# Kernel tuning notes

Hardware: AMD Instinct MI355X
Metric: run time of the kernel (lower is better)

Reference implementation:

```python
import jax, jax.numpy as jnp
import numpy as np

# dimensions
B, NQ, D, H, L, KT, KF = 4, 8192, 256, 8, 4, 2, 2
K = KT * KF
DH = D // H
SPATIAL = np.array([[64, 64], [32, 32], [16, 16], [8, 8]], dtype=np.int32)  # (H_l, W_l)
_sizes = SPATIAL[:, 0] * SPATIAL[:, 1]
LSI = np.concatenate([[0], np.cumsum(_sizes)[:-1]]).astype(np.int32)
NV = int(_sizes.sum())


def setup_inputs() -> dict:
    key = jax.random.key(0)
    ks = jax.random.split(key, 12)
    s = 0.02  # small weight scale keeps tanh in linear region like the zero-init original
    # biases per _reset_parameters: +-0.5 grid for offsets, level-specialization for level_weights
    b_time = jnp.asarray(np.tile(np.linspace(-0.5, 0.5, KT), H * L).astype(np.float32))
    b_freq = jnp.asarray(np.tile(np.linspace(-0.5, 0.5, KF).astype(np.float32), H * L))
    lvl_bias = np.zeros((H, L), dtype=np.float32)
    hpl = max(1, H // L)
    for lvl in range(L):
        lvl_bias[lvl * hpl:min(lvl * hpl + hpl, H), lvl] = 1.0
    return dict(
        query=jax.random.normal(ks[0], (B, NQ, D), jnp.float32),
        reference_points=jax.random.uniform(ks[1], (B, NQ, L, 2), jnp.float32),
        value=jax.random.normal(ks[2], (B, NV, D), jnp.float32),
        spatial_shapes=jnp.asarray(SPATIAL),
        level_start_index=jnp.asarray(LSI),
        W_time=jax.random.normal(ks[3], (D, H * L * KT), jnp.float32) * s,
        b_time=b_time,
        W_freq=jax.random.normal(ks[4], (D, H * L * KF), jnp.float32) * s,
        b_freq=b_freq,
        W_lvl=jax.random.normal(ks[5], (D, H * L), jnp.float32) * s,
        b_lvl=jnp.asarray(lvl_bias.reshape(-1)),
        W_pt=jax.random.normal(ks[6], (D, H * L * K), jnp.float32) * s,
        b_pt=jnp.zeros((H * L * K,), jnp.float32),
        W_v=jax.random.normal(ks[7], (D, D), jnp.float32) * (1.0 / np.sqrt(D)),
        b_v=jnp.zeros((D,), jnp.float32),
        W_o=jax.random.normal(ks[8], (D, D), jnp.float32) * (1.0 / np.sqrt(D)),
        b_o=jnp.zeros((D,), jnp.float32),
    )


def _bilinear(vlev, gx, gy, Hl, Wl):
    # vlev: [B,H,Hl*Wl,DH]; gx,gy: [B,H,NQ,K] normalized grid coords in [-1,1]
    # F.grid_sample(align_corners=False, padding_mode='zeros') semantics
    x = (gx + 1.0) * (Wl * 0.5) - 0.5
    y = (gy + 1.0) * (Hl * 0.5) - 0.5
    x0 = jnp.floor(x)
    y0 = jnp.floor(y)
    wx1 = x - x0
    wy1 = y - y0
    x0i = x0.astype(jnp.int32)
    y0i = y0.astype(jnp.int32)

    def gather(xi, yi, w):
        valid = (xi >= 0) & (xi < Wl) & (yi >= 0) & (yi < Hl)
        idx = jnp.clip(yi, 0, Hl - 1) * Wl + jnp.clip(xi, 0, Wl - 1)
        b, h, nq, k = idx.shape
        v = jnp.take_along_axis(vlev, idx.reshape(b, h, nq * k)[..., None], axis=2)
        v = v.reshape(b, h, nq, k, DH)
        return v * (w * valid)[..., None]

    return (gather(x0i, y0i, (1.0 - wx1) * (1.0 - wy1))
            + gather(x0i + 1, y0i, wx1 * (1.0 - wy1))
            + gather(x0i, y0i + 1, (1.0 - wx1) * wy1)
            + gather(x0i + 1, y0i + 1, wx1 * wy1))


def _forward(query, reference_points, value, W_time, b_time, W_freq, b_freq,
             W_lvl, b_lvl, W_pt, b_pt, W_v, b_v, W_o, b_o,
             spatial_shapes, level_start_index):
    ss = np.asarray(spatial_shapes)
    lsi = np.asarray(level_start_index)
    # predicted separable offsets (offset_scale = 1.0)
    t_off = jnp.tanh(query @ W_time + b_time).reshape(B, NQ, H, L, KT)
    f_off = jnp.tanh(query @ W_freq + b_freq).reshape(B, NQ, H, L, KF)
    # square grid: outer product of time (x) and freq (y) offsets -> K = KT*KF points
    off = jnp.stack([
        jnp.broadcast_to(t_off[..., :, None], (B, NQ, H, L, KT, KF)),
        jnp.broadcast_to(f_off[..., None, :], (B, NQ, H, L, KT, KF)),
    ], axis=-1).reshape(B, NQ, H, L, K, 2)
    # normalizer: (W_l, H_l) per level
    norm = jnp.stack([spatial_shapes[:, 1], spatial_shapes[:, 0]], axis=-1).astype(jnp.float32)
    loc = reference_points[:, :, None, :, None, :] + off / norm[None, None, None, :, None, :]
    loc = jnp.clip(loc, 0.0, 1.0)
    grid = 2.0 * loc - 1.0  # [B,NQ,H,L,K,2], last dim = (x, y)
    # attention weights: softmax over levels times softmax over points
    lw = jax.nn.softmax((query @ W_lvl + b_lvl).reshape(B, NQ, H, L), axis=-1)
    pw = jax.nn.softmax((query @ W_pt + b_pt).reshape(B, NQ, H, L, K), axis=-1)
    attn = lw[..., None] * pw  # [B,NQ,H,L,K]
    v = (value @ W_v + b_v).reshape(B, NV, H, DH)
    out = jnp.zeros((B, NQ, H, DH), jnp.float32)
    for lid in range(L):
        Hl, Wl = int(ss[lid, 0]), int(ss[lid, 1])
        start = int(lsi[lid])
        vlev = v[:, start:start + Hl * Wl].transpose(0, 2, 1, 3)  # [B,H,S_l,DH]
        gx = grid[:, :, :, lid, :, 0].transpose(0, 2, 1, 3)  # [B,H,NQ,K]
        gy = grid[:, :, :, lid, :, 1].transpose(0, 2, 1, 3)
        sampled = _bilinear(vlev, gx, gy, Hl, Wl)  # [B,H,NQ,K,DH]
        a = attn[:, :, :, lid, :].transpose(0, 2, 1, 3)  # [B,H,NQ,K]
        out = out + jnp.einsum('bhqkd,bhqk->bqhd', sampled, a)
    out = out.reshape(B, NQ, D)
    return out @ W_o + b_o


def reference(query, reference_points, value, spatial_shapes, level_start_index,
              W_time, b_time, W_freq, b_freq, W_lvl, b_lvl, W_pt, b_pt,
              W_v, b_v, W_o, b_o):
    return _forward(query, reference_points, value, W_time, b_time, W_freq, b_freq,
                    W_lvl, b_lvl, W_pt, b_pt, W_v, b_v, W_o, b_o,
                    spatial_shapes, level_start_index)
```

## Files before the change

kernel.cpp:

```cpp
#include <hip/hip_runtime.h>
#include <math.h>

#define B_  4
#define NQ_ 8192
#define D_  256
#define H_  8
#define L_  4
#define K_  4
#define DH_ 32
#define NV_ 5440

#define SLAB_ 5936

typedef short bf16x8 __attribute__((ext_vector_type(8)));
typedef float f32x4  __attribute__((ext_vector_type(4)));
typedef unsigned short u16x8 __attribute__((ext_vector_type(8)));

__device__ __forceinline__ ushort f2bf(float f) {
    union { float f; unsigned u; } v; v.f = f;
    return (ushort)((v.u + 0x7FFF + ((v.u >> 16) & 1)) >> 16);
}
__device__ __forceinline__ float bf2f(ushort u) {
    union { unsigned u; float f; } v; v.u = ((unsigned)u) << 16;
    return v.f;
}

__global__ __launch_bounds__(256) void k_zero(uint4* __restrict__ p) {
    p[(size_t)blockIdx.x * 256 + threadIdx.x] = make_uint4(0, 0, 0, 0);
}

__global__ __launch_bounds__(256) void k_cvta(const float* __restrict__ in,
                                              ushort* __restrict__ out) {
    const size_t base = ((size_t)blockIdx.x * 256 + threadIdx.x) * 8;
    const float4 a = *(const float4*)(in + base);
    const float4 b = *(const float4*)(in + base + 4);
    u16x8 u;
    u[0] = f2bf(a.x); u[1] = f2bf(a.y); u[2] = f2bf(a.z); u[3] = f2bf(a.w);
    u[4] = f2bf(b.x); u[5] = f2bf(b.y); u[6] = f2bf(b.z); u[7] = f2bf(b.w);
    *(u16x8*)(out + base) = u;
}

__global__ __launch_bounds__(256) void k_cvtw(const float* __restrict__ in,
                                              ushort* __restrict__ out) {
    const int n = blockIdx.x, k = threadIdx.x;
    out[n * 256 + k] = f2bf(in[k * 256 + n]);
}

__global__ __launch_bounds__(256) void k_cvtwq(const float* __restrict__ Wt,
                                               const float* __restrict__ Wf,
                                               const float* __restrict__ Wlv,
                                               const float* __restrict__ Wp,
                                               ushort* __restrict__ out) {
    const int n = blockIdx.x, k = threadIdx.x;
    float v;
    if (n < 64)       v = Wt[k * 64 + n];
    else if (n < 128) v = Wf[k * 64 + (n - 64)];
    else if (n < 160) v = Wlv[k * 32 + (n - 128)];
    else              v = Wp[k * 128 + (n - 160)];
    out[n * 256 + k] = f2bf(v);
}

template<int NT, int MODE, int AF32>
__global__ __launch_bounds__(256) void k_gemm(const void* __restrict__ Ap,
                                              const ushort* __restrict__ Bt,
                                              const float* __restrict__ bias,
                                              void* __restrict__ Cp) {
    constexpr int NFN = NT / 32;
    __shared__ ushort As[128 * 32];
    __shared__ ushort Bs[NT * 32];
    const int m0   = blockIdx.x * 128;
    const int n0   = blockIdx.y * NT;
    const int t    = threadIdx.x;
    const int w    = t >> 6;
    const int lane = t & 63;
    const int wm   = (w >> 1) * 64;
    const int wn   = (w & 1) * (NT / 2);
    const int lm   = lane & 15;
    const int quad = lane >> 4;

    f32x4 acc[4][NFN];
    #pragma unroll
    for (int i = 0; i < 4; ++i)
        #pragma unroll
        for (int j = 0; j < NFN; ++j)
            acc[i][j] = (f32x4)(0.f);

    for (int kc = 0; kc < 256; kc += 32) {
        __syncthreads();
        if (AF32) {
            const float* A = (const float*)Ap;
            #pragma unroll
            for (int i = 0; i < 4; ++i) {
                const int c   = t + i * 256;
                const int row = c >> 3, ko = (c & 7) * 4;
                const float4 v = *(const float4*)&A[(size_t)(m0 + row) * 256 + kc + ko];
                ushort4 u; u.x = f2bf(v.x); u.y = f2bf(v.y); u.z = f2bf(v.z); u.w = f2bf(v.w);
                *(ushort4*)&As[row * 32 + ko] = u;
            }
        } else {
            const ushort* A = (const ushort*)Ap;
            #pragma unroll
            for (int i = 0; i < 2; ++i) {
                const int c   = t + i * 256;
                const int row = c >> 2, ko = (c & 3) * 8;
                *(u16x8*)&As[row * 32 + ko] =
                    *(const u16x8*)&A[(size_t)(m0 + row) * 256 + kc + ko];
            }
        }
        #pragma unroll
        for (int i = 0; i < 2; ++i) {
            const int c = t + i * 256;
            if (NT == 128 || c < NT * 4) {
                const int row = c >> 2, ko = (c & 3) * 8;
                *(u16x8*)&Bs[row * 32 + ko] =
                    *(const u16x8*)&Bt[(size_t)(n0 + row) * 256 + kc + ko];
            }
        }
        __syncthreads();

        bf16x8 af[4], bfr[NFN];
        #pragma unroll
        for (int mf = 0; mf < 4; ++mf)
            af[mf] = *(const bf16x8*)&As[(wm + mf * 16 + lm) * 32 + quad * 8];
        #pragma unroll
        for (int nf = 0; nf < NFN; ++nf)
            bfr[nf] = *(const bf16x8*)&Bs[(wn + nf * 16 + lm) * 32 + quad * 8];
        #pragma unroll
        for (int mf = 0; mf < 4; ++mf)
            #pragma unroll
            for (int nf = 0; nf < NFN; ++nf)
                acc[mf][nf] = __builtin_amdgcn_mfma_f32_16x16x32_bf16(
                    af[mf], bfr[nf], acc[mf][nf], 0, 0, 0);
    }

    #pragma unroll
    for (int mf = 0; mf < 4; ++mf) {
        #pragma unroll
        for (int nf = 0; nf < NFN; ++nf) {
            const f32x4 a = acc[mf][nf];
            const int col   = n0 + wn + nf * 16 + lm;
            const int rbase = m0 + wm + mf * 16 + quad * 4;
            #pragma unroll
            for (int r = 0; r < 4; ++r) {
                const int row = rbase + r;
                const float v = a[r];
                if (MODE == 0) {
                    ((float*)Cp)[(size_t)row * 256 + col] = v + bias[col];
                } else if (MODE == 1) {
                    const int b = row / NV_, s = row - b * NV_;
                    const int h = col >> 5, dh = col & 31;
                    const int l = (s >= 5376) ? 3 : (s >= 5120) ? 2 : (s >= 4096) ? 1 : 0;
                    const int lsi_[4] = {0, 4096, 5120, 5376};
                    const int po_[4]  = {0, 4356, 5512, 5836};
                    const int o  = s - lsi_[l];
                    const int Wl = 64 >> l;
                    const int y  = o >> (6 - l);
                    const int x  = o & (Wl - 1);
                    const int prow = po_[l] + (y + 1) * (Wl + 2) + (x + 1);
                    ((ushort*)Cp)[(((size_t)(b * H_ + h)) * SLAB_ + prow) * 32 + dh] =
                        f2bf(v + bias[col]);
                } else {
                    ((float*)Cp)[(size_t)row * 288 + col] = v;
                }
            }
        }
    }
}

__global__ __launch_bounds__(256) void k_epi(const float* __restrict__ logits,
                                             const float* __restrict__ refpts,
                                             const float* __restrict__ bt,
                                             const float* __restrict__ bfq,
                                             const float* __restrict__ blv,
                                             const float* __restrict__ bp,
                                             float* __restrict__ params) {
    const int item = blockIdx.x * 256 + threadIdx.x;
    const int qg = item >> 5;
    const int hl = item & 31;
    const int h = hl >> 2, l = hl & 3;
    const float* lgr = logits + (size_t)qg * 288;

    const float tA = tanhf(lgr[hl * 2 + 0] + bt[hl * 2 + 0]);
    const float tB = tanhf(lgr[hl * 2 + 1] + bt[hl * 2 + 1]);
    const float fA = tanhf(lgr[64 + hl * 2 + 0] + bfq[hl * 2 + 0]);
    const float fB = tanhf(lgr[64 + hl * 2 + 1] + bfq[hl * 2 + 1]);

    const float l0 = lgr[128 + h * 4 + 0] + blv[h * 4 + 0];
    const float l1 = lgr[128 + h * 4 + 1] + blv[h * 4 + 1];
    const float l2 = lgr[128 + h * 4 + 2] + blv[h * 4 + 2];
    const float l3 = lgr[128 + h * 4 + 3] + blv[h * 4 + 3];
    const float lm = fmaxf(fmaxf(l0, l1), fmaxf(l2, l3));
    const float e0 = __expf(l0 - lm), e1 = __expf(l1 - lm);
    const float e2 = __expf(l2 - lm), e3 = __expf(l3 - lm);
    const float lsum = e0 + e1 + e2 + e3;
    const float lwv = ((l == 0) ? e0 : (l == 1) ? e1 : (l == 2) ? e2 : e3) / lsum;

    const float p0 = lgr[160 + hl * 4 + 0] + bp[hl * 4 + 0];
    const float p1 = lgr[160 + hl * 4 + 1] + bp[hl * 4 + 1];
    const float p2 = lgr[160 + hl * 4 + 2] + bp[hl * 4 + 2];
    const float p3 = lgr[160 + hl * 4 + 3] + bp[hl * 4 + 3];
    const float pmx = fmaxf(fmaxf(p0, p1), fmaxf(p2, p3));
    const float q0e = __expf(p0 - pmx), q1e = __expf(p1 - pmx);
    const float q2e = __expf(p2 - pmx), q3e = __expf(p3 - pmx);
    const float inv = lwv / (q0e + q1e + q2e + q3e);

    const float rx = refpts[((size_t)qg * L_ + l) * 2 + 0];
    const float ry = refpts[((size_t)qg * L_ + l) * 2 + 1];
    const float Wlf = (float)(64 >> l);
    const float Hlf = (float)(64 >> l);
    const float xA = fminf(fmaxf(rx + tA / Wlf, 0.f), 1.f) * Wlf - 0.5f;
    const float xB = fminf(fmaxf(rx + tB / Wlf, 0.f), 1.f) * Wlf - 0.5f;
    const float yA = fminf(fmaxf(ry + fA / Hlf, 0.f), 1.f) * Hlf - 0.5f;
    const float yB = fminf(fmaxf(ry + fB / Hlf, 0.f), 1.f) * Hlf - 0.5f;

    float* pp = params + (size_t)qg * 256 + hl * 8;
    pp[0] = q0e * inv; pp[1] = q1e * inv; pp[2] = q2e * inv; pp[3] = q3e * inv;
    pp[4] = xA; pp[5] = xB; pp[6] = yA; pp[7] = yB;
}

__global__ __launch_bounds__(256) void k_sample(const ushort* __restrict__ vperm,
                                                const float* __restrict__ params,
                                                ushort* __restrict__ mid) {
    __shared__ float pm[8][264];
    const int b   = blockIdx.y;
    const int q0  = blockIdx.x * 8;
    const int t   = threadIdx.x;
    const int qs  = t >> 6;
    const int sub = t & 63;
    const int h   = sub >> 3;
    const int dh4 = sub & 7;

    for (int i = t; i < 8 * 256; i += 256) {
        const int q = i >> 8, c = i & 255;
        pm[q][(c >> 5) * 33 + (c & 31)] = params[((size_t)(b * NQ_ + q0 + q)) * 256 + c];
    }
    __syncthreads();

    const ushort* vb = vperm + ((size_t)(b * H_ + h)) * SLAB_ * 32 + dh4 * 4;
    const int po_[4] = {0, 4356, 5512, 5836};

    #pragma unroll
    for (int i = 0; i < 2; ++i) {
        const int ql = qs + i * 4;
        f32x4 acc = (f32x4)(0.f);
        #pragma unroll
        for (int l = 0; l < L_; ++l) {
            const int W2 = (64 >> l) + 2;
            const ushort* vl = vb + (size_t)po_[l] * 32;
            const float* p  = &pm[ql][h * 33 + l * 8];
            const float a0 = p[0], a1 = p[1], a2 = p[2], a3 = p[3];
            const float xA = p[4], xB = p[5], yA = p[6], yB = p[7];
            const float xa0 = floorf(xA), xb0 = floorf(xB);
            const float ya0 = floorf(yA), yb0 = floorf(yB);
            const float fxa = xA - xa0, fxb = xB - xb0;
            const float fya = yA - ya0, fyb = yB - yb0;
            const int pxa = (int)xa0 + 1, pxb = (int)xb0 + 1;
            const int pya = (int)ya0 + 1, pyb = (int)yb0 + 1;
            #pragma unroll
            for (int k = 0; k < 4; ++k) {
                const int   px = (k & 2) ? pxb : pxa;
                const int   py = (k & 1) ? pyb : pya;
                const float fx = (k & 2) ? fxb : fxa;
                const float fy = (k & 1) ? fyb : fya;
                const float ak = (k == 0) ? a0 : (k == 1) ? a1 : (k == 2) ? a2 : a3;
                const ushort* c = vl + (size_t)(py * W2 + px) * 32;
                const ushort4 u00 = *(const ushort4*)c;
                const ushort4 u10 = *(const ushort4*)(c + 32);
                const ushort4 u01 = *(const ushort4*)(c + W2 * 32);
                const ushort4 u11 = *(const ushort4*)(c + (W2 + 1) * 32);
                const float gx = 1.f - fx, gy = 1.f - fy;
                const float w00 = ak * gx * gy, w10 = ak * fx * gy;
                const float w01 = ak * gx * fy, w11 = ak * fx * fy;
                f32x4 v;
                v.x = bf2f(u00.x) * w00 + bf2f(u10.x) * w10 + bf2f(u01.x) * w01 + bf2f(u11.x) * w11;
                v.y = bf2f(u00.y) * w00 + bf2f(u10.y) * w10 + bf2f(u01.y) * w01 + bf2f(u11.y) * w11;
                v.z = bf2f(u00.z) * w00 + bf2f(u10.z) * w10 + bf2f(u01.z) * w01 + bf2f(u11.z) * w11;
                v.w = bf2f(u00.w) * w00 + bf2f(u10.w) * w10 + bf2f(u01.w) * w01 + bf2f(u11.w) * w11;
                acc += v;
            }
        }
        ushort4 o;
        o.x = f2bf(acc.x); o.y = f2bf(acc.y); o.z = f2bf(acc.z); o.w = f2bf(acc.w);
        *(ushort4*)&mid[((size_t)(b * NQ_ + q0 + ql)) * 256 + sub * 4] = o;
    }
}

extern "C" void kernel_launch(void* const* d_in, const int* in_sizes, int n_in,
                              void* d_out, int out_size, void* d_ws, size_t ws_size,
                              hipStream_t stream) {
    const float* query = (const float*)d_in[0];
    const float* refp  = (const float*)d_in[1];
    const float* value = (const float*)d_in[2];
    const float* Wt = (const float*)d_in[5];
    const float* bt = (const float*)d_in[6];
    const float* Wf = (const float*)d_in[7];
    const float* bf = (const float*)d_in[8];
    const float* Wl = (const float*)d_in[9];
    const float* bl = (const float*)d_in[10];
    const float* Wp = (const float*)d_in[11];
    const float* bp = (const float*)d_in[12];
    const float* Wv = (const float*)d_in[13];
    const float* bv = (const float*)d_in[14];
    const float* Wo = (const float*)d_in[15];
    const float* bo = (const float*)d_in[16];

    char* wsb = (char*)d_ws;
    ushort* vperm  = (ushort*)wsb;
    float*  params = (float*)(wsb + 12156928);
    ushort* qbf    = (ushort*)(wsb + 12156928);
    float*  logits = (float*)(wsb + 45711360);
    ushort* midb   = (ushort*)(wsb + 45711360);
    ushort* Wvt    = (ushort*)(wsb + 83460096);
    ushort* Wot    = (ushort*)(wsb + 83591168);
    ushort* Wqt    = (ushort*)(wsb + 83722240);

    k_cvtw<<<256, 256, 0, stream>>>(Wv, Wvt);
    k_cvtw<<<256, 256, 0, stream>>>(Wo, Wot);
    k_cvtwq<<<288, 256, 0, stream>>>(Wt, Wf, Wl, Wp, Wqt);
    k_cvta<<<4096, 256, 0, stream>>>(query, qbf);
    k_zero<<<2968, 256, 0, stream>>>((uint4*)vperm);

    k_gemm<128, 1, 1><<<dim3(170, 2), 256, 0, stream>>>(value, Wvt, bv, vperm);
    k_gemm<96, 2, 0><<<dim3(256, 3), 256, 0, stream>>>(qbf, Wqt, nullptr, logits);
    k_epi<<<4096, 256, 0, stream>>>(logits, refp, bt, bf, bl, bp, params);
    k_sample<<<dim3(NQ_ / 8, B_), 256, 0, stream>>>(vperm, params, midb);
    k_gemm<128, 0, 0><<<dim3(256, 2), 256, 0, stream>>>(midb, Wot, bo, (float*)d_out);
}
```

Baseline: 260.4 us.

## Fuse query projection with epilogue, merge prep kernels, widen sampling vectors

Merges the weight conversions and zeroing into one prep kernel, and fuses the query cast, query projection GEMM and softmax/offset epilogue into a single kernel that stages logits in shared memory. This removes the bf16 query buffer and the fp32 logits round trip through global memory, plus several launches. The sampling kernel now has each thread handle 8 channels of one query with 16-byte loads and declares an occupancy hint of 5 blocks. The fused projection uses 64-row tiles with 18 accumulators per wave, which raises register pressure and could lower occupancy.

```diff
diff --git a/kernel.cpp b/kernel.cpp
--- a/kernel.cpp
+++ b/kernel.cpp
@@ -14,6 +14,7 @@
 
 typedef short bf16x8 __attribute__((ext_vector_type(8)));
 typedef float f32x4  __attribute__((ext_vector_type(4)));
+typedef float f32x8  __attribute__((ext_vector_type(8)));
 typedef unsigned short u16x8 __attribute__((ext_vector_type(8)));
 
 __device__ __forceinline__ ushort f2bf(float f) {
@@ -25,47 +26,43 @@
     return v.f;
 }
 
-__global__ __launch_bounds__(256) void k_zero(uint4* __restrict__ p) {
-    p[(size_t)blockIdx.x * 256 + threadIdx.x] = make_uint4(0, 0, 0, 0);
-}
-
-__global__ __launch_bounds__(256) void k_cvta(const float* __restrict__ in,
-                                              ushort* __restrict__ out) {
-    const size_t base = ((size_t)blockIdx.x * 256 + threadIdx.x) * 8;
-    const float4 a = *(const float4*)(in + base);
-    const float4 b = *(const float4*)(in + base + 4);
-    u16x8 u;
-    u[0] = f2bf(a.x); u[1] = f2bf(a.y); u[2] = f2bf(a.z); u[3] = f2bf(a.w);
-    u[4] = f2bf(b.x); u[5] = f2bf(b.y); u[6] = f2bf(b.z); u[7] = f2bf(b.w);
-    *(u16x8*)(out + base) = u;
-}
-
-__global__ __launch_bounds__(256) void k_cvtw(const float* __restrict__ in,
-                                              ushort* __restrict__ out) {
-    const int n = blockIdx.x, k = threadIdx.x;
-    out[n * 256 + k] = f2bf(in[k * 256 + n]);
-}
-
-__global__ __launch_bounds__(256) void k_cvtwq(const float* __restrict__ Wt,
-                                               const float* __restrict__ Wf,
-                                               const float* __restrict__ Wlv,
-                                               const float* __restrict__ Wp,
-                                               ushort* __restrict__ out) {
-    const int n = blockIdx.x, k = threadIdx.x;
-    float v;
-    if (n < 64)       v = Wt[k * 64 + n];
-    else if (n < 128) v = Wf[k * 64 + (n - 64)];
-    else if (n < 160) v = Wlv[k * 32 + (n - 128)];
-    else              v = Wp[k * 128 + (n - 160)];
-    out[n * 256 + k] = f2bf(v);
-}
-
-template<int NT, int MODE, int AF32>
+__global__ __launch_bounds__(256) void k_prep(const float* __restrict__ Wv,
+                                              const float* __restrict__ Wo,
+                                              const float* __restrict__ Wt,
+                                              const float* __restrict__ Wf,
+                                              const float* __restrict__ Wlv,
+                                              const float* __restrict__ Wp,
+                                              uint4* __restrict__ vzero,
+                                              ushort* __restrict__ Wvt,
+                                              ushort* __restrict__ Wot,
+                                              ushort* __restrict__ Wqt) {
+    const int bk = blockIdx.x;
+    const int t  = threadIdx.x;
+    if (bk < 2968) {
+        vzero[(size_t)bk * 256 + t] = make_uint4(0, 0, 0, 0);
+    } else if (bk < 3480) {
+        const float* in; ushort* out; int n;
+        if (bk < 3224) { in = Wv; out = Wvt; n = bk - 2968; }
+        else           { in = Wo; out = Wot; n = bk - 3224; }
+        out[n * 256 + t] = f2bf(in[t * 256 + n]);
+    } else {
+        const int n = bk - 3480;
+        float v;
+        if (n < 64)       v = Wt[t * 64 + n];
+        else if (n < 128) v = Wf[t * 64 + (n - 64)];
+        else if (n < 160) v = Wlv[t * 32 + (n - 128)];
+        else              v = Wp[t * 128 + (n - 160)];
+        Wqt[n * 256 + t] = f2bf(v);
+    }
+}
+
+template<int MODE, int AF32>
 __global__ __launch_bounds__(256) void k_gemm(const void* __restrict__ Ap,
                                               const ushort* __restrict__ Bt,
                                               const float* __restrict__ bias,
                                               void* __restrict__ Cp) {
-    constexpr int NFN = NT / 32;
+    constexpr int NT = 128;
+    constexpr int NFN = 4;
     __shared__ ushort As[128 * 32];
     __shared__ ushort Bs[NT * 32];
     const int m0   = blockIdx.x * 128;
@@ -110,11 +107,9 @@
         #pragma unroll
         for (int i = 0; i < 2; ++i) {
             const int c = t + i * 256;
-            if (NT == 128 || c < NT * 4) {
-                const int row = c >> 2, ko = (c & 3) * 8;
-                *(u16x8*)&Bs[row * 32 + ko] =
-                    *(const u16x8*)&Bt[(size_t)(n0 + row) * 256 + kc + ko];
-            }
+            const int row = c >> 2, ko = (c & 3) * 8;
+            *(u16x8*)&Bs[row * 32 + ko] =
+                *(const u16x8*)&Bt[(size_t)(n0 + row) * 256 + kc + ko];
         }
         __syncthreads();
 
@@ -146,7 +141,7 @@
                 const float v = a[r];
                 if (MODE == 0) {
                     ((float*)Cp)[(size_t)row * 256 + col] = v + bias[col];
-                } else if (MODE == 1) {
+                } else {
                     const int b = row / NV_, s = row - b * NV_;
                     const int h = col >> 5, dh = col & 31;
                     const int l = (s >= 5376) ? 3 : (s >= 5120) ? 2 : (s >= 4096) ? 1 : 0;
@@ -159,76 +154,151 @@
                     const int prow = po_[l] + (y + 1) * (Wl + 2) + (x + 1);
                     ((ushort*)Cp)[(((size_t)(b * H_ + h)) * SLAB_ + prow) * 32 + dh] =
                         f2bf(v + bias[col]);
-                } else {
-                    ((float*)Cp)[(size_t)row * 288 + col] = v;
                 }
             }
         }
     }
 }
 
-__global__ __launch_bounds__(256) void k_epi(const float* __restrict__ logits,
-                                             const float* __restrict__ refpts,
-                                             const float* __restrict__ bt,
-                                             const float* __restrict__ bfq,
-                                             const float* __restrict__ blv,
-                                             const float* __restrict__ bp,
-                                             float* __restrict__ params) {
-    const int item = blockIdx.x * 256 + threadIdx.x;
-    const int qg = item >> 5;
-    const int hl = item & 31;
-    const int h = hl >> 2, l = hl & 3;
-    const float* lgr = logits + (size_t)qg * 288;
-
-    const float tA = tanhf(lgr[hl * 2 + 0] + bt[hl * 2 + 0]);
-    const float tB = tanhf(lgr[hl * 2 + 1] + bt[hl * 2 + 1]);
-    const float fA = tanhf(lgr[64 + hl * 2 + 0] + bfq[hl * 2 + 0]);
-    const float fB = tanhf(lgr[64 + hl * 2 + 1] + bfq[hl * 2 + 1]);
-
-    const float l0 = lgr[128 + h * 4 + 0] + blv[h * 4 + 0];
-    const float l1 = lgr[128 + h * 4 + 1] + blv[h * 4 + 1];
-    const float l2 = lgr[128 + h * 4 + 2] + blv[h * 4 + 2];
-    const float l3 = lgr[128 + h * 4 + 3] + blv[h * 4 + 3];
-    const float lm = fmaxf(fmaxf(l0, l1), fmaxf(l2, l3));
-    const float e0 = __expf(l0 - lm), e1 = __expf(l1 - lm);
-    const float e2 = __expf(l2 - lm), e3 = __expf(l3 - lm);
-    const float lsum = e0 + e1 + e2 + e3;
-    const float lwv = ((l == 0) ? e0 : (l == 1) ? e1 : (l == 2) ? e2 : e3) / lsum;
-
-    const float p0 = lgr[160 + hl * 4 + 0] + bp[hl * 4 + 0];
-    const float p1 = lgr[160 + hl * 4 + 1] + bp[hl * 4 + 1];
-    const float p2 = lgr[160 + hl * 4 + 2] + bp[hl * 4 + 2];
-    const float p3 = lgr[160 + hl * 4 + 3] + bp[hl * 4 + 3];
-    const float pmx = fmaxf(fmaxf(p0, p1), fmaxf(p2, p3));
-    const float q0e = __expf(p0 - pmx), q1e = __expf(p1 - pmx);
-    const float q2e = __expf(p2 - pmx), q3e = __expf(p3 - pmx);
-    const float inv = lwv / (q0e + q1e + q2e + q3e);
-
-    const float rx = refpts[((size_t)qg * L_ + l) * 2 + 0];
-    const float ry = refpts[((size_t)qg * L_ + l) * 2 + 1];
-    const float Wlf = (float)(64 >> l);
-    const float Hlf = (float)(64 >> l);
-    const float xA = fminf(fmaxf(rx + tA / Wlf, 0.f), 1.f) * Wlf - 0.5f;
-    const float xB = fminf(fmaxf(rx + tB / Wlf, 0.f), 1.f) * Wlf - 0.5f;
-    const float yA = fminf(fmaxf(ry + fA / Hlf, 0.f), 1.f) * Hlf - 0.5f;
-    const float yB = fminf(fmaxf(ry + fB / Hlf, 0.f), 1.f) * Hlf - 0.5f;
-
-    float* pp = params + (size_t)qg * 256 + hl * 8;
-    pp[0] = q0e * inv; pp[1] = q1e * inv; pp[2] = q2e * inv; pp[3] = q3e * inv;
-    pp[4] = xA; pp[5] = xB; pp[6] = yA; pp[7] = yB;
-}
-
-__global__ __launch_bounds__(256) void k_sample(const ushort* __restrict__ vperm,
-                                                const float* __restrict__ params,
-                                                ushort* __restrict__ mid) {
+__global__ __launch_bounds__(256) void k_qproj(const float* __restrict__ query,
+                                               const ushort* __restrict__ Wqt,
+                                               const float* __restrict__ refpts,
+                                               const float* __restrict__ bt,
+                                               const float* __restrict__ bfq,
+                                               const float* __restrict__ blv,
+                                               const float* __restrict__ bp,
+                                               float* __restrict__ params) {
+    __shared__ __align__(16) char smem[37888];
+    ushort* As = (ushort*)smem;
+    ushort* Bs = As + 64 * 32;
+    float*  ep = (float*)smem;
+
+    const int m0   = blockIdx.x * 64;
+    const int t    = threadIdx.x;
+    const int w    = t >> 6;
+    const int lane = t & 63;
+    const int wm   = (w >> 1) * 32;
+    const int wn   = (w & 1) * 144;
+    const int lm   = lane & 15;
+    const int quad = lane >> 4;
+
+    f32x4 acc[2][9];
+    #pragma unroll
+    for (int i = 0; i < 2; ++i)
+        #pragma unroll
+        for (int j = 0; j < 9; ++j)
+            acc[i][j] = (f32x4)(0.f);
+
+    for (int kc = 0; kc < 256; kc += 32) {
+        __syncthreads();
+        #pragma unroll
+        for (int i = 0; i < 2; ++i) {
+            const int c   = t + i * 256;
+            const int row = c >> 3, ko = (c & 7) * 4;
+            const float4 v = *(const float4*)&query[(size_t)(m0 + row) * 256 + kc + ko];
+            ushort4 u; u.x = f2bf(v.x); u.y = f2bf(v.y); u.z = f2bf(v.z); u.w = f2bf(v.w);
+            *(ushort4*)&As[row * 32 + ko] = u;
+        }
+        #pragma unroll
+        for (int i = 0; i < 5; ++i) {
+            const int c = t + i * 256;
+            if (c < 1152) {
+                const int row = c >> 2, ko = (c & 3) * 8;
+                *(u16x8*)&Bs[row * 32 + ko] =
+                    *(const u16x8*)&Wqt[(size_t)row * 256 + kc + ko];
+            }
+        }
+        __syncthreads();
+
+        bf16x8 af[2], bfr[9];
+        #pragma unroll
+        for (int mf = 0; mf < 2; ++mf)
+            af[mf] = *(const bf16x8*)&As[(wm + mf * 16 + lm) * 32 + quad * 8];
+        #pragma unroll
+        for (int nf = 0; nf < 9; ++nf)
+            bfr[nf] = *(const bf16x8*)&Bs[(wn + nf * 16 + lm) * 32 + quad * 8];
+        #pragma unroll
+        for (int mf = 0; mf < 2; ++mf)
+            #pragma unroll
+            for (int nf = 0; nf < 9; ++nf)
+                acc[mf][nf] = __builtin_amdgcn_mfma_f32_16x16x32_bf16(
+                    af[mf], bfr[nf], acc[mf][nf], 0, 0, 0);
+    }
+
+    #pragma unroll
+    for (int ph = 0; ph < 2; ++ph) {
+        __syncthreads();
+        if ((w >> 1) == ph) {
+            #pragma unroll
+            for (int mf = 0; mf < 2; ++mf)
+                #pragma unroll
+                for (int nf = 0; nf < 9; ++nf)
+                    #pragma unroll
+                    for (int r = 0; r < 4; ++r)
+                        ep[(mf * 16 + quad * 4 + r) * 296 + wn + nf * 16 + lm]
+                            = acc[mf][nf][r];
+        }
+        __syncthreads();
+        #pragma unroll
+        for (int it = 0; it < 4; ++it) {
+            const int item = t + it * 256;
+            const int qr = item >> 5;
+            const int hl = item & 31;
+            const int h = hl >> 2, l = hl & 3;
+            const int qg = m0 + ph * 32 + qr;
+            const float* lgr = &ep[qr * 296];
+
+            const float tA = tanhf(lgr[hl * 2 + 0] + bt[hl * 2 + 0]);
+            const float tB = tanhf(lgr[hl * 2 + 1] + bt[hl * 2 + 1]);
+            const float fA = tanhf(lgr[64 + hl * 2 + 0] + bfq[hl * 2 + 0]);
+            const float fB = tanhf(lgr[64 + hl * 2 + 1] + bfq[hl * 2 + 1]);
+
+            const float l0 = lgr[128 + h * 4 + 0] + blv[h * 4 + 0];
+            const float l1 = lgr[128 + h * 4 + 1] + blv[h * 4 + 1];
+            const float l2 = lgr[128 + h * 4 + 2] + blv[h * 4 + 2];
+            const float l3 = lgr[128 + h * 4 + 3] + blv[h * 4 + 3];
+            const float lmx = fmaxf(fmaxf(l0, l1), fmaxf(l2, l3));
+            const float e0 = __expf(l0 - lmx), e1 = __expf(l1 - lmx);
+            const float e2 = __expf(l2 - lmx), e3 = __expf(l3 - lmx);
+            const float lsum = e0 + e1 + e2 + e3;
+            const float lwv = ((l == 0) ? e0 : (l == 1) ? e1 : (l == 2) ? e2 : e3) / lsum;
+
+            const float p0 = lgr[160 + hl * 4 + 0] + bp[hl * 4 + 0];
+            const float p1 = lgr[160 + hl * 4 + 1] + bp[hl * 4 + 1];
+            const float p2 = lgr[160 + hl * 4 + 2] + bp[hl * 4 + 2];
+            const float p3 = lgr[160 + hl * 4 + 3] + bp[hl * 4 + 3];
+            const float pmx = fmaxf(fmaxf(p0, p1), fmaxf(p2, p3));
+            const float q0e = __expf(p0 - pmx), q1e = __expf(p1 - pmx);
+            const float q2e = __expf(p2 - pmx), q3e = __expf(p3 - pmx);
+            const float inv = lwv / (q0e + q1e + q2e + q3e);
+
+            const float rx = refpts[((size_t)qg * L_ + l) * 2 + 0];
+            const float ry = refpts[((size_t)qg * L_ + l) * 2 + 1];
+            const float Wlf = (float)(64 >> l);
+            const float Hlf = (float)(64 >> l);
+            const float xA = fminf(fmaxf(rx + tA / Wlf, 0.f), 1.f) * Wlf - 0.5f;
+            const float xB = fminf(fmaxf(rx + tB / Wlf, 0.f), 1.f) * Wlf - 0.5f;
+            const float yA = fminf(fmaxf(ry + fA / Hlf, 0.f), 1.f) * Hlf - 0.5f;
+            const float yB = fminf(fmaxf(ry + fB / Hlf, 0.f), 1.f) * Hlf - 0.5f;
+
+            float* pp = params + (size_t)qg * 256 + hl * 8;
+            pp[0] = q0e * inv; pp[1] = q1e * inv; pp[2] = q2e * inv; pp[3] = q3e * inv;
+            pp[4] = xA; pp[5] = xB; pp[6] = yA; pp[7] = yB;
+        }
+    }
+}
+
+__global__ __launch_bounds__(256, 5) void k_sample(const ushort* __restrict__ vperm,
+                                                   const float* __restrict__ params,
+                                                   ushort* __restrict__ mid) {
     __shared__ float pm[8][264];
     const int b   = blockIdx.y;
     const int q0  = blockIdx.x * 8;
     const int t   = threadIdx.x;
-    const int qs  = t >> 6;
-    const int sub = t & 63;
-    const int h   = sub >> 3;
-    const int dh4 = sub & 7;
+    const int ql  = t >> 5;
+    const int sub = t & 31;
+    const int h   = sub >> 2;
+    const int dh8 = sub & 3;
 
     for (int i = t; i < 8 * 256; i += 256) {
         const int q = i >> 8, c = i & 255;
@@ -236,53 +306,48 @@
     }
     __syncthreads();
 
-    const ushort* vb = vperm + ((size_t)(b * H_ + h)) * SLAB_ * 32 + dh4 * 4;
+    const ushort* vb = vperm + ((size_t)(b * H_ + h)) * SLAB_ * 32 + dh8 * 8;
     const int po_[4] = {0, 4356, 5512, 5836};
 
-    #pragma unroll
-    for (int i = 0; i < 2; ++i) {
-        const int ql = qs + i * 4;
-        f32x4 acc = (f32x4)(0.f);
-        #pragma unroll
-        for (int l = 0; l < L_; ++l) {
-            const int W2 = (64 >> l) + 2;
-            const ushort* vl = vb + (size_t)po_[l] * 32;
-            const float* p  = &pm[ql][h * 33 + l * 8];
-            const float a0 = p[0], a1 = p[1], a2 = p[2], a3 = p[3];
-            const float xA = p[4], xB = p[5], yA = p[6], yB = p[7];
-            const float xa0 = floorf(xA), xb0 = floorf(xB);
-            const float ya0 = floorf(yA), yb0 = floorf(yB);
-            const float fxa = xA - xa0, fxb = xB - xb0;
-            const float fya = yA - ya0, fyb = yB - yb0;
-            const int pxa = (int)xa0 + 1, pxb = (int)xb0 + 1;
-            const int pya = (int)ya0 + 1, pyb = (int)yb0 + 1;
-            #pragma unroll
-            for (int k = 0; k < 4; ++k) {
-                const int   px = (k & 2) ? pxb : pxa;
-                const int   py = (k & 1) ? pyb : pya;
-                const float fx = (k & 2) ? fxb : fxa;
-                const float fy = (k & 1) ? fyb : fya;
-                const float ak = (k == 0) ? a0 : (k == 1) ? a1 : (k == 2) ? a2 : a3;
-                const ushort* c = vl + (size_t)(py * W2 + px) * 32;
-                const ushort4 u00 = *(const ushort4*)c;
-                const ushort4 u10 = *(const ushort4*)(c + 32);
-                const ushort4 u01 = *(const ushort4*)(c + W2 * 32);
-                const ushort4 u11 = *(const ushort4*)(c + (W2 + 1) * 32);
-                const float gx = 1.f - fx, gy = 1.f - fy;
-                const float w00 = ak * gx * gy, w10 = ak * fx * gy;
-                const float w01 = ak * gx * fy, w11 = ak * fx * fy;
-                f32x4 v;
-                v.x = bf2f(u00.x) * w00 + bf2f(u10.x) * w10 + bf2f(u01.x) * w01 + bf2f(u11.x) * w11;
-                v.y = bf2f(u00.y) * w00 + bf2f(u10.y) * w10 + bf2f(u01.y) * w01 + bf2f(u11.y) * w11;
-                v.z = bf2f(u00.z) * w00 + bf2f(u10.z) * w10 + bf2f(u01.z) * w01 + bf2f(u11.z) * w11;
-                v.w = bf2f(u00.w) * w00 + bf2f(u10.w) * w10 + bf2f(u01.w) * w01 + bf2f(u11.w) * w11;
-                acc += v;
-            }
-        }
-        ushort4 o;
-        o.x = f2bf(acc.x); o.y = f2bf(acc.y); o.z = f2bf(acc.z); o.w = f2bf(acc.w);
-        *(ushort4*)&mid[((size_t)(b * NQ_ + q0 + ql)) * 256 + sub * 4] = o;
-    }
+    f32x8 acc = (f32x8)(0.f);
+    #pragma unroll
+    for (int l = 0; l < L_; ++l) {
+        const int W2 = (64 >> l) + 2;
+        const ushort* vl = vb + (size_t)po_[l] * 32;
+        const float* p  = &pm[ql][h * 33 + l * 8];
+        const float a0 = p[0], a1 = p[1], a2 = p[2], a3 = p[3];
+        const float xA = p[4], xB = p[5], yA = p[6], yB = p[7];
+        const float xa0 = floorf(xA), xb0 = floorf(xB);
+        const float ya0 = floorf(yA), yb0 = floorf(yB);
+        const float fxa = xA - xa0, fxb = xB - xb0;
+        const float fya = yA - ya0, fyb = yB - yb0;
+        const int pxa = (int)xa0 + 1, pxb = (int)xb0 + 1;
+        const int pya = (int)ya0 + 1, pyb = (int)yb0 + 1;
+        #pragma unroll
+        for (int k = 0; k < 4; ++k) {
+            const int   px = (k & 2) ? pxb : pxa;
+            const int   py = (k & 1) ? pyb : pya;
+            const float fx = (k & 2) ? fxb : fxa;
+            const float fy = (k & 1) ? fyb : fya;
+            const float ak = (k == 0) ? a0 : (k == 1) ? a1 : (k == 2) ? a2 : a3;
+            const ushort* cp = vl + (size_t)(py * W2 + px) * 32;
+            const u16x8 u00 = *(const u16x8*)cp;
+            const u16x8 u10 = *(const u16x8*)(cp + 32);
+            const u16x8 u01 = *(const u16x8*)(cp + W2 * 32);
+            const u16x8 u11 = *(const u16x8*)(cp + (W2 + 1) * 32);
+            const float gx = 1.f - fx, gy = 1.f - fy;
+            const float w00 = ak * gx * gy, w10 = ak * fx * gy;
+            const float w01 = ak * gx * fy, w11 = ak * fx * fy;
+            #pragma unroll
+            for (int e = 0; e < 8; ++e)
+                acc[e] += bf2f(u00[e]) * w00 + bf2f(u10[e]) * w10
+                        + bf2f(u01[e]) * w01 + bf2f(u11[e]) * w11;
+        }
+    }
+    u16x8 o;
+    #pragma unroll
+    for (int e = 0; e < 8; ++e) o[e] = f2bf(acc[e]);
+    *(u16x8*)&mid[((size_t)(b * NQ_ + q0 + ql)) * 256 + sub * 8] = o;
 }
 
 extern "C" void kernel_launch(void* const* d_in, const int* in_sizes, int n_in,
@@ -307,22 +372,15 @@
     char* wsb = (char*)d_ws;
     ushort* vperm  = (ushort*)wsb;
     float*  params = (float*)(wsb + 12156928);
-    ushort* qbf    = (ushort*)(wsb + 12156928);
-    float*  logits = (float*)(wsb + 45711360);
     ushort* midb   = (ushort*)(wsb + 45711360);
-    ushort* Wvt    = (ushort*)(wsb + 83460096);
-    ushort* Wot    = (ushort*)(wsb + 83591168);
-    ushort* Wqt    = (ushort*)(wsb + 83722240);
-
-    k_cvtw<<<256, 256, 0, stream>>>(Wv, Wvt);
-    k_cvtw<<<256, 256, 0, stream>>>(Wo, Wot);
-    k_cvtwq<<<288, 256, 0, stream>>>(Wt, Wf, Wl, Wp, Wqt);
-    k_cvta<<<4096, 256, 0, stream>>>(query, qbf);
-    k_zero<<<2968, 256, 0, stream>>>((uint4*)vperm);
-
-    k_gemm<128, 1, 1><<<dim3(170, 2), 256, 0, stream>>>(value, Wvt, bv, vperm);
-    k_gemm<96, 2, 0><<<dim3(256, 3), 256, 0, stream>>>(qbf, Wqt, nullptr, logits);
-    k_epi<<<4096, 256, 0, stream>>>(logits, refp, bt, bf, bl, bp, params);
+    ushort* Wvt    = (ushort*)(wsb + 62488576);
+    ushort* Wot    = (ushort*)(wsb + 62619648);
+    ushort* Wqt    = (ushort*)(wsb + 62750720);
+
+    k_prep<<<3768, 256, 0, stream>>>(Wv, Wo, Wt, Wf, Wl, Wp,
+                                     (uint4*)vperm, Wvt, Wot, Wqt);
+    k_gemm<1, 1><<<dim3(170, 2), 256, 0, stream>>>(value, Wvt, bv, vperm);
+    k_qproj<<<512, 256, 0, stream>>>(query, Wqt, refp, bt, bf, bl, bp, params);
     k_sample<<<dim3(NQ_ / 8, B_), 256, 0, stream>>>(vperm, params, midb);
-    k_gemm<128, 0, 0><<<dim3(256, 2), 256, 0, stream>>>(midb, Wot, bo, (float*)d_out);
-}
+    k_gemm<0, 0><<<dim3(256, 2), 256, 0, stream>>>(midb, Wot, bo, (float*)d_out);
+}
```

Measured after the change: 484.1 us. +85.9%, slower.
